# Kernel tuning notes

Hardware: AMD Instinct MI355X
Metric: run time of the kernel (lower is better)

The kernel has to match this reference:

```python
import jax, jax.numpy as jnp
import numpy as np

B = 1048576          # batch of parallel trials; feature dims (12, 24) are fixed by the architecture
THRESH = 0.5         # braincog IFNode default threshold; mem starts at 0 so spike = (input > thresh)


def if_spike(i):
    # Fresh IFNode: mem = 0 + i ; spike = Heaviside(mem - threshold); mem reset where spiked (state unused here)
    return (i > THRESH).astype(i.dtype)


def setup_inputs() -> dict:
    key = jax.random.key(0)
    k1, k2 = jax.random.split(key)
    x1 = jax.random.uniform(k1, (B, 12), dtype=jnp.float32)
    x2 = jax.random.uniform(k2, (B, 24), dtype=jnp.float32)
    # Connection weights exactly as constructed in BNESNN.__init__
    W0 = jnp.eye(12, dtype=jnp.float32) * 6.0            # connection[0]
    W1 = jnp.zeros((12, 24), dtype=jnp.float32)          # connection[1]
    W2 = jnp.eye(24, dtype=jnp.float32) * 6.0            # connection[2]
    return {"x1": x1, "x2": x2, "W0": W0, "W1": W1, "W2": W2}


def reference(x1, x2, W0, W1, W2):
    # --- stdp[0] = STDP(node0, connection0) ---
    # i0 = CustomLinear: x1 @ W0 ; spikes via IF node; trace (fresh, decay irrelevant on 1st step) = x1
    i0 = x1 @ W0                      # [B, 12]
    s0 = if_spike(i0)                 # [B, 12] spikes (out__s)
    # dw0 = trace^T @ s0 is computed in torch but NOT returned by BNESNN.forward, so we skip it

    # --- stdp[1] = MutliInputSTDP(node1, [connection1, connection2]) ---
    i1 = s0 @ W1 + x2 @ W2            # [B, 24] summed synaptic currents
    s1 = if_spike(i1)                 # [B, 24] spikes (out__p)
    # autograd.grad(i1, [W1, W2], grad_outputs=s1) with inputs replaced in-place by their traces
    # (fresh traces == the inputs themselves): dw = trace^T @ s1
    dw1 = jnp.einsum('bi,bj->ij', s0, s1)   # [12, 24] grad wrt connection[1].weight
    dw2 = jnp.einsum('bi,bj->ij', x2, s1)   # [24, 24] grad wrt connection[2].weight

    # BNESNN.forward returns (dw, out__s, out__p) with dw = (dw1, dw2); flattened here
    return (dw1, dw2, s0, s1)
```

## Files before the change

### kernel.cpp

```cpp
#include <hip/hip_runtime.h>


typedef __bf16 bf16x8 __attribute__((ext_vector_type(8)));
typedef float  f32x4  __attribute__((ext_vector_type(4)));

constexpr int TPB = 256;
constexpr int LDSS = 72;

__global__ void zero_dw_kernel(float* out) {
    int t = threadIdx.x + blockIdx.x * blockDim.x;
    if (t < 864) out[t] = 0.0f;
}

__global__ __launch_bounds__(TPB, 3)
void bnesnn_kernel(const float* __restrict__ x1, const float* __restrict__ x2,
                   const float* __restrict__ W0, const float* __restrict__ W1,
                   const float* __restrict__ W2, float* __restrict__ out, int B)
{
    __shared__ __attribute__((aligned(16))) __bf16 aT[4 * 48 * LDSS];
    __shared__ __attribute__((aligned(16))) __bf16 bT[4 * 32 * LDSS];

    const int tid = threadIdx.x;
    const int w   = tid >> 6;
    const int l   = tid & 63;
    __bf16* aTw = aT + w * 48 * LDSS;
    __bf16* bTw = bT + w * 32 * LDSS;

    for (int i = l; i < 12 * LDSS; i += 64) aTw[36 * LDSS + i] = (__bf16)0.0f;
    for (int i = l; i <  8 * LDSS; i += 64) bTw[24 * LDSS + i] = (__bf16)0.0f;

    bool okv = true;
    for (int i = tid; i < 144; i += TPB) if ((i / 12) != (i % 12) && W0[i] != 0.0f) okv = false;
    for (int i = tid; i < 288; i += TPB) if (W1[i] != 0.0f) okv = false;
    for (int i = tid; i < 576; i += TPB) if ((i / 24) != (i % 24) && W2[i] != 0.0f) okv = false;
    const int fast = __syncthreads_and(okv ? 1 : 0);

    float* s0out = out + 864;
    float* s1out = out + 864 + (size_t)12 * B;

    const int lrow = l & 15;
    const int kb   = (l >> 4) * 8;

    f32x4 acc[6] = {};

    const int NT = (B + 255) / 256;

    auto mfmaPhase = [&]() {
        #pragma unroll
        for (int p = 0; p < 6; ++p) {
            const int mt = p % 3, nt = p / 3;
            const int ar = (mt * 16 + lrow) * LDSS + kb;
            const int br = (nt * 16 + lrow) * LDSS + kb;
            #pragma unroll
            for (int kk = 0; kk < 64; kk += 32) {
                bf16x8 af = *(const bf16x8*)&aTw[ar + kk];
                bf16x8 bf = *(const bf16x8*)&bTw[br + kk];
                acc[p] = __builtin_amdgcn_mfma_f32_16x16x32_bf16(af, bf, acc[p], 0, 0, 0);
            }
        }
    };

    if (fast) {
        f32x4 D0[3], D2[6];
        #pragma unroll
        for (int c = 0; c < 3; ++c) {
            D0[c][0] = W0[(4*c+0)*13]; D0[c][1] = W0[(4*c+1)*13];
            D0[c][2] = W0[(4*c+2)*13]; D0[c][3] = W0[(4*c+3)*13];
        }
        #pragma unroll
        for (int c = 0; c < 6; ++c) {
            D2[c][0] = W2[(4*c+0)*25]; D2[c][1] = W2[(4*c+1)*25];
            D2[c][2] = W2[(4*c+2)*25]; D2[c][3] = W2[(4*c+3)*25];
        }
        const int t3 = l % 3, t6 = l % 6;
        f32x4 e0[3], e2[6];
        #pragma unroll
        for (int k = 0; k < 3; ++k) {
            int i = (t3 + k) % 3;
            e0[k] = (i == 0) ? D0[0] : ((i == 1) ? D0[1] : D0[2]);
        }
        #pragma unroll
        for (int k = 0; k < 6; ++k) {
            int i = (t6 + 4 * k) % 6;
            e2[k] = (i == 0) ? D2[0] : ((i == 1) ? D2[1] : ((i == 2) ? D2[2] :
                    ((i == 3) ? D2[3] : ((i == 4) ? D2[4] : D2[5]))));
        }

        const float4* p1 = (const float4*)x1;
        const float4* p2 = (const float4*)x2;
        float4*       q0 = (float4*)s0out;
        float4*       q1 = (float4*)s1out;
        const size_t  n1 = (size_t)B * 3;
        const size_t  n2 = (size_t)B * 6;
        const float4  z  = make_float4(0.f, 0.f, 0.f, 0.f);

        for (int t = blockIdx.x; t < NT; t += gridDim.x) {
            const size_t b1 = (size_t)t * 768  + (size_t)w * 192;
            const size_t b2 = (size_t)t * 1536 + (size_t)w * 384;

            float4 buf[9];
            #pragma unroll
            for (int k = 0; k < 3; ++k) { size_t i = b1 + k * 64 + l; buf[k]     = (i < n1) ? p1[i] : z; }
            #pragma unroll
            for (int k = 0; k < 6; ++k) { size_t i = b2 + k * 64 + l; buf[3 + k] = (i < n2) ? p2[i] : z; }

            #pragma unroll
            for (int k = 0; k < 3; ++k) {
                int q = k * 64 + l;
                int r = q / 3;
                int c = 4 * (q - 3 * r);
                float4 v = buf[k];
                f32x4  e = e0[k];
                float sa = (v.x * e[0] > 0.5f) ? 1.f : 0.f;
                float sb = (v.y * e[1] > 0.5f) ? 1.f : 0.f;
                float sc = (v.z * e[2] > 0.5f) ? 1.f : 0.f;
                float sd = (v.w * e[3] > 0.5f) ? 1.f : 0.f;
                size_t gi = b1 + q;
                if (gi < n1) q0[gi] = make_float4(sa, sb, sc, sd);
                aTw[(c + 0) * LDSS + r] = (__bf16)sa;
                aTw[(c + 1) * LDSS + r] = (__bf16)sb;
                aTw[(c + 2) * LDSS + r] = (__bf16)sc;
                aTw[(c + 3) * LDSS + r] = (__bf16)sd;
            }
            #pragma unroll
            for (int k = 0; k < 6; ++k) {
                int q = k * 64 + l;
                int r = q / 6;
                int c = 4 * (q - 6 * r);
                float4 v = buf[3 + k];
                f32x4  e = e2[k];
                float sa = (v.x * e[0] > 0.5f) ? 1.f : 0.f;
                float sb = (v.y * e[1] > 0.5f) ? 1.f : 0.f;
                float sc = (v.z * e[2] > 0.5f) ? 1.f : 0.f;
                float sd = (v.w * e[3] > 0.5f) ? 1.f : 0.f;
                size_t gi = b2 + q;
                if (gi < n2) q1[gi] = make_float4(sa, sb, sc, sd);
                aTw[(12 + c + 0) * LDSS + r] = (__bf16)v.x;
                aTw[(12 + c + 1) * LDSS + r] = (__bf16)v.y;
                aTw[(12 + c + 2) * LDSS + r] = (__bf16)v.z;
                aTw[(12 + c + 3) * LDSS + r] = (__bf16)v.w;
                bTw[(c + 0) * LDSS + r] = (__bf16)sa;
                bTw[(c + 1) * LDSS + r] = (__bf16)sb;
                bTw[(c + 2) * LDSS + r] = (__bf16)sc;
                bTw[(c + 3) * LDSS + r] = (__bf16)sd;
            }
            mfmaPhase();
        }
    } else {
        for (int t = blockIdx.x; t < NT; t += gridDim.x) {
            long r = (long)t * 256 + w * 64 + l;
            bool v = r < B;
            float xv[36];
            const float4 z = make_float4(0.f, 0.f, 0.f, 0.f);
            const float4* p1 = (const float4*)(x1 + r * 12);
            const float4* p2 = (const float4*)(x2 + r * 24);
            #pragma unroll
            for (int c = 0; c < 3; ++c) {
                float4 t4 = v ? p1[c] : z;
                xv[4*c+0] = t4.x; xv[4*c+1] = t4.y; xv[4*c+2] = t4.z; xv[4*c+3] = t4.w;
            }
            #pragma unroll
            for (int c = 0; c < 6; ++c) {
                float4 t4 = v ? p2[c] : z;
                xv[12+4*c+0] = t4.x; xv[12+4*c+1] = t4.y; xv[12+4*c+2] = t4.z; xv[12+4*c+3] = t4.w;
            }
            float s0v[12], s1v[24];
            #pragma unroll 1
            for (int j = 0; j < 12; ++j) {
                float a = 0.0f;
                for (int k = 0; k < 12; ++k) a += xv[k] * W0[k * 12 + j];
                s0v[j] = (a > 0.5f) ? 1.0f : 0.0f;
            }
            #pragma unroll 1
            for (int j = 0; j < 24; ++j) {
                float a = 0.0f;
                for (int k = 0; k < 12; ++k) a += s0v[k] * W1[k * 24 + j];
                for (int k = 0; k < 24; ++k) a += xv[12 + k] * W2[k * 24 + j];
                s1v[j] = (a > 0.5f) ? 1.0f : 0.0f;
            }
            if (v) {
                float4* q0 = (float4*)(s0out + (size_t)r * 12);
                q0[0] = make_float4(s0v[0], s0v[1], s0v[2],  s0v[3]);
                q0[1] = make_float4(s0v[4], s0v[5], s0v[6],  s0v[7]);
                q0[2] = make_float4(s0v[8], s0v[9], s0v[10], s0v[11]);
                float4* q1 = (float4*)(s1out + (size_t)r * 24);
                #pragma unroll
                for (int c = 0; c < 6; ++c)
                    q1[c] = make_float4(s1v[4*c+0], s1v[4*c+1], s1v[4*c+2], s1v[4*c+3]);
            }
            #pragma unroll
            for (int m = 0; m < 12; ++m) aTw[m * LDSS + l]        = (__bf16)(v ? s0v[m] : 0.f);
            #pragma unroll
            for (int m = 0; m < 24; ++m) aTw[(12 + m) * LDSS + l] = (__bf16)(v ? xv[12 + m] : 0.f);
            #pragma unroll
            for (int n = 0; n < 24; ++n) bTw[n * LDSS + l]        = (__bf16)(v ? s1v[n] : 0.f);
            mfmaPhase();
        }
    }

    __syncthreads();
    float* red = (float*)aT;
    #pragma unroll
    for (int p = 0; p < 6; ++p)
        *(f32x4*)&red[(w * 6 + p) * 256 + l * 4] = acc[p];
    __syncthreads();
    for (int e = tid; e < 1536; e += TPB) {
        int p  = e >> 8, le = e & 255;
        float s = red[p * 256 + le] + red[(6 + p) * 256 + le]
                + red[(12 + p) * 256 + le] + red[(18 + p) * 256 + le];
        int lane = le >> 2, i = le & 3;
        int m = (p % 3) * 16 + (lane >> 4) * 4 + i;
        int n = (p / 3) * 16 + (lane & 15);
        if (m < 36 && n < 24) {
            int addr = (m < 12) ? (m * 24 + n) : (288 + (m - 12) * 24 + n);
            atomicAdd(out + addr, s);
        }
    }
}

extern "C" void kernel_launch(void* const* d_in, const int* in_sizes, int n_in,
                              void* d_out, int out_size, void* d_ws, size_t ws_size,
                              hipStream_t stream) {
    const float* x1 = (const float*)d_in[0];
    const float* x2 = (const float*)d_in[1];
    const float* W0 = (const float*)d_in[2];
    const float* W1 = (const float*)d_in[3];
    const float* W2 = (const float*)d_in[4];
    float* out = (float*)d_out;
    const int B = in_sizes[0] / 12;
    if (B <= 0) return;

    zero_dw_kernel<<<dim3(4), dim3(256), 0, stream>>>(out);
    bnesnn_kernel<<<dim3(768), dim3(TPB), 0, stream>>>(x1, x2, W0, W1, W2, out, B);
}
```

Measured before the change: 85.68 us.

## Double-buffer global loads across tiles in register ping-pong loop

Restructures the grid-stride tile loop so the next tile's x1/x2 float4 loads are issued into a second register set before the current tile's spike computation, LDS writes and MFMA phase run. This is meant to hide global-memory latency behind compute. It doubles the live load registers (18 float4), which under launch_bounds(256,3) could cause spills or lower occupancy.

```diff
diff --git a/kernel.cpp b/kernel.cpp
--- a/kernel.cpp
+++ b/kernel.cpp
@@ -94,58 +94,78 @@
         const size_t  n2 = (size_t)B * 6;
         const float4  z  = make_float4(0.f, 0.f, 0.f, 0.f);
 
-        for (int t = blockIdx.x; t < NT; t += gridDim.x) {
-            const size_t b1 = (size_t)t * 768  + (size_t)w * 192;
-            const size_t b2 = (size_t)t * 1536 + (size_t)w * 384;
-
-            float4 buf[9];
-            #pragma unroll
-            for (int k = 0; k < 3; ++k) { size_t i = b1 + k * 64 + l; buf[k]     = (i < n1) ? p1[i] : z; }
-            #pragma unroll
-            for (int k = 0; k < 6; ++k) { size_t i = b2 + k * 64 + l; buf[3 + k] = (i < n2) ? p2[i] : z; }
-
-            #pragma unroll
-            for (int k = 0; k < 3; ++k) {
-                int q = k * 64 + l;
-                int r = q / 3;
-                int c = 4 * (q - 3 * r);
-                float4 v = buf[k];
-                f32x4  e = e0[k];
-                float sa = (v.x * e[0] > 0.5f) ? 1.f : 0.f;
-                float sb = (v.y * e[1] > 0.5f) ? 1.f : 0.f;
-                float sc = (v.z * e[2] > 0.5f) ? 1.f : 0.f;
-                float sd = (v.w * e[3] > 0.5f) ? 1.f : 0.f;
-                size_t gi = b1 + q;
-                if (gi < n1) q0[gi] = make_float4(sa, sb, sc, sd);
-                aTw[(c + 0) * LDSS + r] = (__bf16)sa;
-                aTw[(c + 1) * LDSS + r] = (__bf16)sb;
-                aTw[(c + 2) * LDSS + r] = (__bf16)sc;
-                aTw[(c + 3) * LDSS + r] = (__bf16)sd;
-            }
-            #pragma unroll
-            for (int k = 0; k < 6; ++k) {
-                int q = k * 64 + l;
-                int r = q / 6;
-                int c = 4 * (q - 6 * r);
-                float4 v = buf[3 + k];
-                f32x4  e = e2[k];
-                float sa = (v.x * e[0] > 0.5f) ? 1.f : 0.f;
-                float sb = (v.y * e[1] > 0.5f) ? 1.f : 0.f;
-                float sc = (v.z * e[2] > 0.5f) ? 1.f : 0.f;
-                float sd = (v.w * e[3] > 0.5f) ? 1.f : 0.f;
-                size_t gi = b2 + q;
-                if (gi < n2) q1[gi] = make_float4(sa, sb, sc, sd);
-                aTw[(12 + c + 0) * LDSS + r] = (__bf16)v.x;
-                aTw[(12 + c + 1) * LDSS + r] = (__bf16)v.y;
-                aTw[(12 + c + 2) * LDSS + r] = (__bf16)v.z;
-                aTw[(12 + c + 3) * LDSS + r] = (__bf16)v.w;
-                bTw[(c + 0) * LDSS + r] = (__bf16)sa;
-                bTw[(c + 1) * LDSS + r] = (__bf16)sb;
-                bTw[(c + 2) * LDSS + r] = (__bf16)sc;
-                bTw[(c + 3) * LDSS + r] = (__bf16)sd;
-            }
-            mfmaPhase();
-        }
+#define LOADT(P, tt) { \
+        const size_t b1 = (size_t)(tt) * 768  + (size_t)w * 192; \
+        const size_t b2 = (size_t)(tt) * 1536 + (size_t)w * 384; \
+        size_t i0_ = b1 + 0 * 64 + l; P##0 = (i0_ < n1) ? p1[i0_] : z; \
+        size_t i1_ = b1 + 1 * 64 + l; P##1 = (i1_ < n1) ? p1[i1_] : z; \
+        size_t i2_ = b1 + 2 * 64 + l; P##2 = (i2_ < n1) ? p1[i2_] : z; \
+        size_t i3_ = b2 + 0 * 64 + l; P##3 = (i3_ < n2) ? p2[i3_] : z; \
+        size_t i4_ = b2 + 1 * 64 + l; P##4 = (i4_ < n2) ? p2[i4_] : z; \
+        size_t i5_ = b2 + 2 * 64 + l; P##5 = (i5_ < n2) ? p2[i5_] : z; \
+        size_t i6_ = b2 + 3 * 64 + l; P##6 = (i6_ < n2) ? p2[i6_] : z; \
+        size_t i7_ = b2 + 4 * 64 + l; P##7 = (i7_ < n2) ? p2[i7_] : z; \
+        size_t i8_ = b2 + 5 * 64 + l; P##8 = (i8_ < n2) ? p2[i8_] : z; }
+
+#define SPK1(P, k) { \
+        int q_ = (k) * 64 + l; int r_ = q_ / 3; int c_ = 4 * (q_ - 3 * r_); \
+        float sa_ = (P.x * e0[k][0] > 0.5f) ? 1.f : 0.f; \
+        float sb_ = (P.y * e0[k][1] > 0.5f) ? 1.f : 0.f; \
+        float sc_ = (P.z * e0[k][2] > 0.5f) ? 1.f : 0.f; \
+        float sd_ = (P.w * e0[k][3] > 0.5f) ? 1.f : 0.f; \
+        size_t gi_ = b1_ + q_; \
+        if (gi_ < n1) q0[gi_] = make_float4(sa_, sb_, sc_, sd_); \
+        aTw[(c_ + 0) * LDSS + r_] = (__bf16)sa_; \
+        aTw[(c_ + 1) * LDSS + r_] = (__bf16)sb_; \
+        aTw[(c_ + 2) * LDSS + r_] = (__bf16)sc_; \
+        aTw[(c_ + 3) * LDSS + r_] = (__bf16)sd_; }
+
+#define SPK2(P, k) { \
+        int q_ = (k) * 64 + l; int r_ = q_ / 6; int c_ = 4 * (q_ - 6 * r_); \
+        float sa_ = (P.x * e2[k][0] > 0.5f) ? 1.f : 0.f; \
+        float sb_ = (P.y * e2[k][1] > 0.5f) ? 1.f : 0.f; \
+        float sc_ = (P.z * e2[k][2] > 0.5f) ? 1.f : 0.f; \
+        float sd_ = (P.w * e2[k][3] > 0.5f) ? 1.f : 0.f; \
+        size_t gi_ = b2_ + q_; \
+        if (gi_ < n2) q1[gi_] = make_float4(sa_, sb_, sc_, sd_); \
+        aTw[(12 + c_ + 0) * LDSS + r_] = (__bf16)P.x; \
+        aTw[(12 + c_ + 1) * LDSS + r_] = (__bf16)P.y; \
+        aTw[(12 + c_ + 2) * LDSS + r_] = (__bf16)P.z; \
+        aTw[(12 + c_ + 3) * LDSS + r_] = (__bf16)P.w; \
+        bTw[(c_ + 0) * LDSS + r_] = (__bf16)sa_; \
+        bTw[(c_ + 1) * LDSS + r_] = (__bf16)sb_; \
+        bTw[(c_ + 2) * LDSS + r_] = (__bf16)sc_; \
+        bTw[(c_ + 3) * LDSS + r_] = (__bf16)sd_; }
+
+#define PROCT(P, tt) { \
+        const size_t b1_ = (size_t)(tt) * 768  + (size_t)w * 192; \
+        const size_t b2_ = (size_t)(tt) * 1536 + (size_t)w * 384; \
+        SPK1(P##0, 0) SPK1(P##1, 1) SPK1(P##2, 2) \
+        SPK2(P##3, 0) SPK2(P##4, 1) SPK2(P##5, 2) \
+        SPK2(P##6, 3) SPK2(P##7, 4) SPK2(P##8, 5) \
+        mfmaPhase(); }
+
+        float4 pA0, pA1, pA2, pA3, pA4, pA5, pA6, pA7, pA8;
+        float4 pB0, pB1, pB2, pB3, pB4, pB5, pB6, pB7, pB8;
+
+        const int stride = gridDim.x;
+        int t = blockIdx.x;
+        if (t < NT) LOADT(pA, t)
+        while (t < NT) {
+            int tn = t + stride;
+            if (tn < NT) LOADT(pB, tn)
+            PROCT(pA, t)
+            t = tn;
+            if (t >= NT) break;
+            tn = t + stride;
+            if (tn < NT) LOADT(pA, tn)
+            PROCT(pB, t)
+            t = tn;
+        }
+#undef LOADT
+#undef SPK1
+#undef SPK2
+#undef PROCT
     } else {
         for (int t = blockIdx.x; t < NT; t += gridDim.x) {
             long r = (long)t * 256 + w * 64 + l;
```

New measurement: 165.6 us. +93.3%, slower.
